# Kernel tuning notes

Hardware: AMD Instinct MI355X
Metric: run time of the kernel (lower is better)

The kernel has to match this reference:

```python
import jax, jax.numpy as jnp
import numpy as np

G = 56      # voxel grid side
N = 60000   # active voxels
K = 27      # 3x3x3 kernel offsets
CIN, COUT = 64, 96


def _build_kernel_map(seed=0):
    """Host-side hash-map neighbor search (what spnn does internally).
    Returns in_idx/out_idx of shape (K, N); padded entries have out_idx == N
    (scattered into a trash row) and in_idx == 0 (any valid gather index)."""
    rng = np.random.default_rng(seed)
    flat = rng.choice(G ** 3, size=N, replace=False)
    coords = np.stack(np.unravel_index(flat, (G, G, G)), axis=1)  # (N, 3)
    lut = -np.ones(G ** 3, dtype=np.int64)
    lut[flat] = np.arange(N)
    offs = np.array([(dx, dy, dz) for dx in (-1, 0, 1)
                     for dy in (-1, 0, 1) for dz in (-1, 0, 1)])
    in_idx = np.zeros((K, N), dtype=np.int32)
    out_idx = np.full((K, N), N, dtype=np.int32)
    for k in range(K):
        nb = coords + offs[k]
        ok = np.all((nb >= 0) & (nb < G), axis=1)
        fl = np.clip(nb[:, 0] * G * G + nb[:, 1] * G + nb[:, 2], 0, G ** 3 - 1)
        j = np.where(ok, lut[fl], -1)
        sel = np.nonzero(j >= 0)[0]
        m = sel.shape[0]
        out_idx[k, :m] = sel.astype(np.int32)       # output point i
        in_idx[k, :m] = j[sel].astype(np.int32)     # its neighbor at offset k
    return jnp.asarray(in_idx), jnp.asarray(out_idx)


def setup_inputs() -> dict:
    key = jax.random.key(0)
    ks = jax.random.split(key, 10)
    in_idx, out_idx = _build_kernel_map(0)
    s1 = 1.0 / np.sqrt(K * CIN)
    s2 = 1.0 / np.sqrt(K * COUT)
    return {
        "x":  jax.random.normal(ks[0], (N, CIN), jnp.float32),
        "W1": jax.random.normal(ks[1], (K, CIN, COUT), jnp.float32) * s1,
        "g1": jnp.ones((COUT,), jnp.float32),
        "b1": jnp.zeros((COUT,), jnp.float32),
        "m1": jax.random.normal(ks[2], (COUT,), jnp.float32) * 0.1,
        "v1": jax.random.uniform(ks[3], (COUT,), jnp.float32, 0.5, 1.5),
        "W2": jax.random.normal(ks[4], (K, COUT, COUT), jnp.float32) * s2,
        "g2": jnp.ones((COUT,), jnp.float32),
        "b2": jnp.zeros((COUT,), jnp.float32),
        "m2": jax.random.normal(ks[5], (COUT,), jnp.float32) * 0.1,
        "v2": jax.random.uniform(ks[6], (COUT,), jnp.float32, 0.5, 1.5),
        "Wd": jax.random.normal(ks[7], (CIN, COUT), jnp.float32) / np.sqrt(CIN),
        "gd": jnp.ones((COUT,), jnp.float32),
        "bd": jnp.zeros((COUT,), jnp.float32),
        "md": jax.random.normal(ks[8], (COUT,), jnp.float32) * 0.1,
        "vd": jax.random.uniform(ks[9], (COUT,), jnp.float32, 0.5, 1.5),
        "in_idx": in_idx,
        "out_idx": out_idx,
    }


def _bn(h, g, b, m, v, eps=1e-5):
    return (h - m) * (g * jax.lax.rsqrt(v + eps)) + b


def _sparse_conv(feat, W, in_idx, out_idx):
    # gather -> GEMM -> scatter-add, one pass per kernel offset.
    n = feat.shape[0]
    out = jnp.zeros((n + 1, W.shape[2]), feat.dtype)  # row n = trash row
    for k in range(W.shape[0]):
        out = out.at[out_idx[k]].add(feat[in_idx[k]] @ W[k])
    return out[:n]


def reference(x, W1, g1, b1, m1, v1, W2, g2, b2, m2, v2,
              Wd, gd, bd, md, vd, in_idx, out_idx):
    h = jax.nn.relu(_bn(_sparse_conv(x, W1, in_idx, out_idx), g1, b1, m1, v1))
    h = _bn(_sparse_conv(h, W2, in_idx, out_idx), g2, b2, m2, v2)
    skip = _bn(x @ Wd, gd, bd, md, vd)  # 1x1 conv downsample (inc != outc)
    return jax.nn.relu(h + skip)
```

## Files before the change

### kernel.cpp

```cpp
#include <hip/hip_runtime.h>


typedef __attribute__((ext_vector_type(8))) short bf16x8;
typedef __attribute__((ext_vector_type(4))) float f32x4;
typedef unsigned short u16;

constexpr int K27  = 27;
constexpr int CIN  = 64;
constexpr int COUT = 96;

#define MFMA __builtin_amdgcn_mfma_f32_16x16x32_bf16

__device__ __forceinline__ u16 f2bf(float f) {
  unsigned u = __float_as_uint(f);
  return (u16)((u + 0x7FFFu + ((u >> 16) & 1u)) >> 16);
}

__device__ __forceinline__ int posf(int c) {
  return ((c >> 2) & 3) * 8 + (c & 3) + ((c >> 4) & 1) * 4;
}

__device__ __forceinline__ bf16x8 ld16(const u16* p) {
  union { bf16x8 f; uint4 u; } r;
  r.u = *reinterpret_cast<const uint4*>(p);
  return r.f;
}

template <int NS>
__device__ __forceinline__ void stageB(const u16* g, u16* l, int t) {
#pragma unroll
  for (int s = 0; s < NS; ++s) {
    __builtin_amdgcn_global_load_lds(
        (const __attribute__((address_space(1))) unsigned int*)(g + s * 2048 + t * 8),
        (__attribute__((address_space(3))) unsigned int*)(l + s * 2048 + t * 8),
        16, 0, 0);
  }
}

__global__ void build_nbT(const int* __restrict__ in_idx, const int* __restrict__ out_idx,
                          int* __restrict__ nbT, int N, int N_pad) {
  int t = blockIdx.x * blockDim.x + threadIdx.x;
  if (t >= K27 * N) return;
  int k = t / N;
  int o = out_idx[t];
  if (o < N) nbT[(size_t)k * N_pad + o] = in_idx[t];
}

__global__ void prep_all(
    const float* __restrict__ x, const float* __restrict__ W1,
    const float* __restrict__ W2, const float* __restrict__ Wd,
    const float* g1, const float* b1, const float* m1, const float* v1,
    const float* g2, const float* b2, const float* m2, const float* v2,
    const float* gd, const float* bd, const float* md, const float* vd,
    u16* __restrict__ xbf, u16* __restrict__ W1t, u16* __restrict__ W2t,
    u16* __restrict__ Wdt, float* __restrict__ bnc, u16* __restrict__ hbf, int N) {
  long i = (long)blockIdx.x * blockDim.x + threadIdx.x;
  const long R0 = (long)(N + 1) * CIN;
  const long R1 = (long)K27 * CIN * COUT;
  const long R2 = (long)K27 * COUT * COUT;
  const long R3 = (long)CIN * COUT;
  if (i < R0) {
    int c = (int)(i & 63);
    float v = (i < (long)N * CIN) ? x[i] : 0.f;
    xbf[(i & ~63L) + (c & 32) + posf(c & 31)] = f2bf(v);
    return;
  }
  i -= R0;
  if (i < R1) {
    int k = (int)(i / (CIN * COUT)), rem = (int)(i % (CIN * COUT));
    int ci = rem / COUT, co = rem % COUT;
    int cidx = (ci & 32) + posf(ci & 31);
    W1t[(size_t)k * 6144 + co * 64 + (cidx ^ ((co & 7) << 3))] = f2bf(W1[i]);
    return;
  }
  i -= R1;
  if (i < R2) {
    int k = (int)(i / (COUT * COUT)), rem = (int)(i % (COUT * COUT));
    int ci = rem / COUT, co = rem % COUT;
    int cidx = (ci >> 5) * 32 + posf(ci & 31);
    W2t[(size_t)k * 12288 + co * 128 + (cidx ^ ((co & 7) << 3))] = f2bf(W2[i]);
    return;
  }
  i -= R2;
  if (i < R3) {
    int ci = (int)(i / COUT), co = (int)(i % COUT);
    Wdt[co * CIN + (ci & 32) + posf(ci & 31)] = f2bf(Wd[i]);
    return;
  }
  i -= R3;
  if (i < COUT) {
    int c = (int)i;
    float A1 = g1[c] * rsqrtf(v1[c] + 1e-5f);
    float A2 = g2[c] * rsqrtf(v2[c] + 1e-5f);
    float Ad = gd[c] * rsqrtf(vd[c] + 1e-5f);
    bnc[c]       = A1;
    bnc[96 + c]  = b1[c] - m1[c] * A1;
    bnc[192 + c] = A2;
    bnc[288 + c] = b2[c] - m2[c] * A2 + bd[c] - md[c] * Ad;
    bnc[384 + c] = Ad / A2;
    hbf[(size_t)N * COUT + c] = 0;
  }
}

__global__ __launch_bounds__(256, 2) void conv1_mfma(
    const u16* __restrict__ xbf, const u16* __restrict__ W1t,
    const int* __restrict__ nbT, const float* __restrict__ bnc,
    u16* __restrict__ hbf, int N, int N_pad) {
  __shared__ u16 Blds[2][6144];
  const int t    = threadIdx.x;
  const int lane = t & 63;
  const int m    = lane & 15;
  const int slot = lane >> 4;
  const int so   = slot * 8;
  const int sw   = (m & 7) << 3;
  const int row0 = blockIdx.x * 64 + (t >> 6) * 16;

  f32x4 acc[6];
#pragma unroll
  for (int n = 0; n < 6; ++n) acc[n] = (f32x4){0.f, 0.f, 0.f, 0.f};

  const int* nbp = nbT + row0 + m;

  stageB<3>(W1t, Blds[0], t);
  int j1 = nbp[N_pad];
  int j2 = nbp[2 * (size_t)N_pad];
  bf16x8 Aa[2], Ab[2];
  {
    int j0 = nbp[0];
    const u16* p = xbf + (size_t)(j0 < 0 ? N : j0) * CIN + so;
    Aa[0] = ld16(p); Aa[1] = ld16(p + 32);
  }
  __syncthreads();

  auto step = [&](int k, bf16x8 (&Ac)[2], bf16x8 (&An)[2]) {
    const int cur = k & 1;
    if (k + 1 < K27) stageB<3>(W1t + (size_t)(k + 1) * 6144, Blds[cur ^ 1], t);
    int jn = j1; j1 = j2;
    j2 = (k + 3 < K27) ? nbp[(size_t)(k + 3) * N_pad] : 0;
    if (k + 1 < K27) {
      const u16* p = xbf + (size_t)(jn < 0 ? N : jn) * CIN + so;
      An[0] = ld16(p); An[1] = ld16(p + 32);
    }
    const u16* Bb = Blds[cur];
#pragma unroll
    for (int c = 0; c < 2; ++c)
#pragma unroll
      for (int n = 0; n < 6; ++n) {
        bf16x8 B = ld16(Bb + n * 1024 + m * 64 + ((c * 32 + so) ^ sw));
        acc[n] = MFMA(Ac[c], B, acc[n], 0, 0, 0);
      }
    __syncthreads();
  };

  for (int kk = 0; kk < K27 - 1; kk += 2) {
    step(kk, Aa, Ab);
    step(kk + 1, Ab, Aa);
  }
  step(K27 - 1, Aa, Ab);

  const int pbase = ((m >> 2) << 3) + (m & 3);
#pragma unroll
  for (int n = 0; n < 6; ++n) {
    const int col  = n * 16 + m;
    const int dcol = (n >> 1) * 32 + pbase + ((n & 1) << 2);
    const float s = bnc[col], b = bnc[COUT + col];
#pragma unroll
    for (int r = 0; r < 4; ++r) {
      const int row = row0 + slot * 4 + r;
      if (row < N)
        hbf[(size_t)row * COUT + dcol] = f2bf(fmaxf(fmaf(acc[n][r], s, b), 0.f));
    }
  }
}

__global__ __launch_bounds__(256, 2) void conv2_mfma(
    const u16* __restrict__ hbf, const u16* __restrict__ W2t,
    const u16* __restrict__ xbf, const u16* __restrict__ Wdt,
    const int* __restrict__ nbT, const float* __restrict__ bnc,
    float* __restrict__ out, int N, int N_pad) {
  __shared__ u16 Blds[2][12288];
  const int t    = threadIdx.x;
  const int lane = t & 63;
  const int m    = lane & 15;
  const int slot = lane >> 4;
  const int so   = slot * 8;
  const int sw   = (m & 7) << 3;
  const int row0 = blockIdx.x * 64 + (t >> 6) * 16;

  f32x4 acc[6];
#pragma unroll
  for (int n = 0; n < 6; ++n) acc[n] = (f32x4){0.f, 0.f, 0.f, 0.f};

  stageB<6>(W2t, Blds[0], t);

  {
    int r0 = row0 + m;
    const u16* p = xbf + (size_t)(r0 < N ? r0 : N) * CIN + so;
    bf16x8 S0 = ld16(p), S1 = ld16(p + 32);
    const u16* wd = Wdt + m * CIN + so;
#pragma unroll
    for (int n = 0; n < 6; ++n) {
      bf16x8 B0 = ld16(wd + n * (16 * CIN));
      bf16x8 B1 = ld16(wd + n * (16 * CIN) + 32);
      acc[n] = MFMA(S0, B0, acc[n], 0, 0, 0);
      acc[n] = MFMA(S1, B1, acc[n], 0, 0, 0);
    }
#pragma unroll
    for (int n = 0; n < 6; ++n) acc[n] *= bnc[384 + n * 16 + m];
  }

  const int* nbp = nbT + row0 + m;
  int j1 = nbp[N_pad];
  int j2 = nbp[2 * (size_t)N_pad];
  bf16x8 Aa[3], Ab[3];
  {
    int j0 = nbp[0];
    const u16* p = hbf + (size_t)(j0 < 0 ? N : j0) * COUT + so;
    Aa[0] = ld16(p); Aa[1] = ld16(p + 32); Aa[2] = ld16(p + 64);
  }
  __syncthreads();

  auto step = [&](int k, bf16x8 (&Ac)[3], bf16x8 (&An)[3]) {
    const int cur = k & 1;
    if (k + 1 < K27) stageB<6>(W2t + (size_t)(k + 1) * 12288, Blds[cur ^ 1], t);
    int jn = j1; j1 = j2;
    j2 = (k + 3 < K27) ? nbp[(size_t)(k + 3) * N_pad] : 0;
    if (k + 1 < K27) {
      const u16* p = hbf + (size_t)(jn < 0 ? N : jn) * COUT + so;
      An[0] = ld16(p); An[1] = ld16(p + 32); An[2] = ld16(p + 64);
    }
    const u16* Bb = Blds[cur];
#pragma unroll
    for (int c = 0; c < 3; ++c)
#pragma unroll
      for (int n = 0; n < 6; ++n) {
        bf16x8 B = ld16(Bb + n * 2048 + m * 128 + ((c * 32 + so) ^ sw));
        acc[n] = MFMA(Ac[c], B, acc[n], 0, 0, 0);
      }
    __syncthreads();
  };

  for (int kk = 0; kk < K27 - 1; kk += 2) {
    step(kk, Aa, Ab);
    step(kk + 1, Ab, Aa);
  }
  step(K27 - 1, Aa, Ab);

#pragma unroll
  for (int n = 0; n < 6; ++n) {
    const int col = n * 16 + m;
    const float s = bnc[192 + col], b = bnc[288 + col];
#pragma unroll
    for (int r = 0; r < 4; ++r) {
      const int row = row0 + slot * 4 + r;
      if (row < N)
        out[(size_t)row * COUT + col] = fmaxf(fmaf(acc[n][r], s, b), 0.f);
    }
  }
}

extern "C" void kernel_launch(void* const* d_in, const int* in_sizes, int n_in,
                              void* d_out, int out_size, void* d_ws, size_t ws_size,
                              hipStream_t stream) {
  const float* x  = (const float*)d_in[0];
  const float* W1 = (const float*)d_in[1];
  const float* g1 = (const float*)d_in[2];
  const float* b1 = (const float*)d_in[3];
  const float* m1 = (const float*)d_in[4];
  const float* v1 = (const float*)d_in[5];
  const float* W2 = (const float*)d_in[6];
  const float* g2 = (const float*)d_in[7];
  const float* b2 = (const float*)d_in[8];
  const float* m2 = (const float*)d_in[9];
  const float* v2 = (const float*)d_in[10];
  const float* Wd = (const float*)d_in[11];
  const float* gd = (const float*)d_in[12];
  const float* bd = (const float*)d_in[13];
  const float* md = (const float*)d_in[14];
  const float* vd = (const float*)d_in[15];
  const int* in_idx  = (const int*)d_in[16];
  const int* out_idx = (const int*)d_in[17];

  const int N  = in_sizes[0] / CIN;
  const int GB = (N + 63) / 64;
  const int N_pad = GB * 64;

  char* ws = (char*)d_ws;
  size_t off = 0;
  auto alloc = [&](size_t bytes) { size_t o = off; off = (off + bytes + 255) & ~(size_t)255; return o; };
  int*   nbT = (int*)(ws + alloc((size_t)K27 * N_pad * sizeof(int)));
  u16*   xbf = (u16*)(ws + alloc((size_t)(N + 1) * CIN * sizeof(u16)));
  u16*   hbf = (u16*)(ws + alloc((size_t)(N + 1) * COUT * sizeof(u16)));
  u16*   W1t = (u16*)(ws + alloc((size_t)K27 * 6144 * sizeof(u16)));
  u16*   W2t = (u16*)(ws + alloc((size_t)K27 * 12288 * sizeof(u16)));
  u16*   Wdt = (u16*)(ws + alloc((size_t)COUT * CIN * sizeof(u16)));
  float* bnc = (float*)(ws + alloc(5 * 96 * sizeof(float)));

  hipMemsetAsync(nbT, 0xFF, (size_t)K27 * N_pad * sizeof(int), stream);
  build_nbT<<<(K27 * N + 255) / 256, 256, 0, stream>>>(in_idx, out_idx, nbT, N, N_pad);

  long ptotal = (long)(N + 1) * CIN + (long)K27 * CIN * COUT +
                (long)K27 * COUT * COUT + (long)CIN * COUT + COUT;
  prep_all<<<(int)((ptotal + 255) / 256), 256, 0, stream>>>(
      x, W1, W2, Wd, g1, b1, m1, v1, g2, b2, m2, v2, gd, bd, md, vd,
      xbf, W1t, W2t, Wdt, bnc, hbf, N);

  conv1_mfma<<<GB, 256, 0, stream>>>(xbf, W1t, nbT, bnc, hbf, N, N_pad);
  conv2_mfma<<<GB, 256, 0, stream>>>(hbf, W2t, xbf, Wdt, nbT, bnc, (float*)d_out, N, N_pad);
}
```

Measured before the change: 125.1 us.

## Retile conv waves to 2x2 grid, prepack weights in MFMA fragment order, XCD-swizzle blocks

Each wave now computes 32 rows by 48 columns instead of 16 rows by 96 columns, so every B fragment read from LDS feeds two MFMAs and LDS traffic per MFMA halves. Weights are prepacked per offset in exact lane-fragment order, removing the XOR swizzle addressing and shrinking W2 staging from 12288 to 9216 elements (no padding). Block indices are remapped across XCDs so neighbouring row blocks share an L2. In exchange, each wave does twice the gather loads per step and holds more registers for A fragments.

```diff
diff --git a/kernel.cpp b/kernel.cpp
--- a/kernel.cpp
+++ b/kernel.cpp
@@ -8,6 +8,8 @@
 constexpr int K27  = 27;
 constexpr int CIN  = 64;
 constexpr int COUT = 96;
+constexpr int W1SZ = 6144;
+constexpr int W2SZ = 9216;
 
 #define MFMA __builtin_amdgcn_mfma_f32_16x16x32_bf16
 
@@ -26,15 +28,27 @@
   return r.f;
 }
 
-template <int NS>
-__device__ __forceinline__ void stageB(const u16* g, u16* l, int t) {
-#pragma unroll
-  for (int s = 0; s < NS; ++s) {
-    __builtin_amdgcn_global_load_lds(
-        (const __attribute__((address_space(1))) unsigned int*)(g + s * 2048 + t * 8),
-        (__attribute__((address_space(3))) unsigned int*)(l + s * 2048 + t * 8),
-        16, 0, 0);
-  }
+__device__ __forceinline__ void gll(const u16* g, u16* l) {
+  __builtin_amdgcn_global_load_lds(
+      (const __attribute__((address_space(1))) unsigned int*)g,
+      (__attribute__((address_space(3))) unsigned int*)l, 16, 0, 0);
+}
+
+__device__ __forceinline__ void stage1(const u16* g, u16* l, int t) {
+#pragma unroll
+  for (int s = 0; s < 3; ++s) gll(g + s * 2048 + t * 8, l + s * 2048 + t * 8);
+}
+
+__device__ __forceinline__ void stage2(const u16* g, u16* l, int t) {
+#pragma unroll
+  for (int s = 0; s < 4; ++s) gll(g + s * 2048 + t * 8, l + s * 2048 + t * 8);
+  if (t < 128) gll(g + 8192 + t * 8, l + 8192 + t * 8);
+}
+
+__device__ __forceinline__ int xcd_swz(int bid, int nblk) {
+  int q = nblk >> 3, r = nblk & 7;
+  int x = bid & 7, i = bid >> 3;
+  return (x < r ? x * (q + 1) : r * (q + 1) + (x - r) * q) + i;
 }
 
 __global__ void build_nbT(const int* __restrict__ in_idx, const int* __restrict__ out_idx,
@@ -56,8 +70,8 @@
     u16* __restrict__ Wdt, float* __restrict__ bnc, u16* __restrict__ hbf, int N) {
   long i = (long)blockIdx.x * blockDim.x + threadIdx.x;
   const long R0 = (long)(N + 1) * CIN;
-  const long R1 = (long)K27 * CIN * COUT;
-  const long R2 = (long)K27 * COUT * COUT;
+  const long R1 = (long)K27 * W1SZ;
+  const long R2 = (long)K27 * W2SZ;
   const long R3 = (long)CIN * COUT;
   if (i < R0) {
     int c = (int)(i & 63);
@@ -67,18 +81,22 @@
   }
   i -= R0;
   if (i < R1) {
-    int k = (int)(i / (CIN * COUT)), rem = (int)(i % (CIN * COUT));
-    int ci = rem / COUT, co = rem % COUT;
-    int cidx = (ci & 32) + posf(ci & 31);
-    W1t[(size_t)k * 6144 + co * 64 + (cidx ^ ((co & 7) << 3))] = f2bf(W1[i]);
+    int k = (int)(i / W1SZ), r = (int)(i % W1SZ);
+    int f = r >> 9, lane = (r >> 3) & 63, j = r & 7;
+    int c = f / 6, n = f % 6, m = lane & 15, g = lane >> 4;
+    int co = n * 16 + m;
+    int ci = c * 32 + 4 * g + (j & 3) + 16 * (j >> 2);
+    W1t[i] = f2bf(W1[((size_t)k * CIN + ci) * COUT + co]);
     return;
   }
   i -= R1;
   if (i < R2) {
-    int k = (int)(i / (COUT * COUT)), rem = (int)(i % (COUT * COUT));
-    int ci = rem / COUT, co = rem % COUT;
-    int cidx = (ci >> 5) * 32 + posf(ci & 31);
-    W2t[(size_t)k * 12288 + co * 128 + (cidx ^ ((co & 7) << 3))] = f2bf(W2[i]);
+    int k = (int)(i / W2SZ), r = (int)(i % W2SZ);
+    int f = r >> 9, lane = (r >> 3) & 63, j = r & 7;
+    int c = f / 6, n = f % 6, m = lane & 15, g = lane >> 4;
+    int co = n * 16 + m;
+    int ci = c * 32 + 4 * g + (j & 3) + 16 * (j >> 2);
+    W2t[i] = f2bf(W2[((size_t)k * COUT + ci) * COUT + co]);
     return;
   }
   i -= R2;
@@ -106,48 +124,62 @@
     const u16* __restrict__ xbf, const u16* __restrict__ W1t,
     const int* __restrict__ nbT, const float* __restrict__ bnc,
     u16* __restrict__ hbf, int N, int N_pad) {
-  __shared__ u16 Blds[2][6144];
+  __shared__ u16 Blds[2][W1SZ];
   const int t    = threadIdx.x;
   const int lane = t & 63;
   const int m    = lane & 15;
   const int slot = lane >> 4;
   const int so   = slot * 8;
-  const int sw   = (m & 7) << 3;
-  const int row0 = blockIdx.x * 64 + (t >> 6) * 16;
-
-  f32x4 acc[6];
-#pragma unroll
-  for (int n = 0; n < 6; ++n) acc[n] = (f32x4){0.f, 0.f, 0.f, 0.f};
-
-  const int* nbp = nbT + row0 + m;
-
-  stageB<3>(W1t, Blds[0], t);
-  int j1 = nbp[N_pad];
-  int j2 = nbp[2 * (size_t)N_pad];
-  bf16x8 Aa[2], Ab[2];
+  const int wid  = t >> 6;
+  const int wr   = wid >> 1;
+  const int wc   = wid & 1;
+  const int bswz = xcd_swz(blockIdx.x, gridDim.x);
+  const int roww = bswz * 64 + wr * 32;
+
+  f32x4 acc[2][3];
+#pragma unroll
+  for (int s = 0; s < 2; ++s)
+#pragma unroll
+    for (int n = 0; n < 3; ++n) acc[s][n] = (f32x4){0.f, 0.f, 0.f, 0.f};
+
+  const int* nbp = nbT + roww + m;
+
+  stage1(W1t, Blds[0], t);
+  int j1a = nbp[N_pad],               j1b = nbp[N_pad + 16];
+  int j2a = nbp[2 * (size_t)N_pad],   j2b = nbp[2 * (size_t)N_pad + 16];
+  bf16x8 Aa[2][2], Ab[2][2];
   {
-    int j0 = nbp[0];
-    const u16* p = xbf + (size_t)(j0 < 0 ? N : j0) * CIN + so;
-    Aa[0] = ld16(p); Aa[1] = ld16(p + 32);
+    int j0a = nbp[0], j0b = nbp[16];
+    const u16* pa = xbf + (size_t)(j0a < 0 ? N : j0a) * CIN + so;
+    const u16* pb = xbf + (size_t)(j0b < 0 ? N : j0b) * CIN + so;
+    Aa[0][0] = ld16(pa); Aa[0][1] = ld16(pa + 32);
+    Aa[1][0] = ld16(pb); Aa[1][1] = ld16(pb + 32);
   }
   __syncthreads();
 
-  auto step = [&](int k, bf16x8 (&Ac)[2], bf16x8 (&An)[2]) {
+  auto step = [&](int k, bf16x8 (&Ac)[2][2], bf16x8 (&An)[2][2]) {
     const int cur = k & 1;
-    if (k + 1 < K27) stageB<3>(W1t + (size_t)(k + 1) * 6144, Blds[cur ^ 1], t);
-    int jn = j1; j1 = j2;
-    j2 = (k + 3 < K27) ? nbp[(size_t)(k + 3) * N_pad] : 0;
+    if (k + 1 < K27) stage1(W1t + (size_t)(k + 1) * W1SZ, Blds[cur ^ 1], t);
+    int j3a = 0, j3b = 0;
+    if (k + 3 < K27) {
+      j3a = nbp[(size_t)(k + 3) * N_pad];
+      j3b = nbp[(size_t)(k + 3) * N_pad + 16];
+    }
     if (k + 1 < K27) {
-      const u16* p = xbf + (size_t)(jn < 0 ? N : jn) * CIN + so;
-      An[0] = ld16(p); An[1] = ld16(p + 32);
-    }
-    const u16* Bb = Blds[cur];
+      const u16* pa = xbf + (size_t)(j1a < 0 ? N : j1a) * CIN + so;
+      const u16* pb = xbf + (size_t)(j1b < 0 ? N : j1b) * CIN + so;
+      An[0][0] = ld16(pa); An[0][1] = ld16(pa + 32);
+      An[1][0] = ld16(pb); An[1][1] = ld16(pb + 32);
+    }
+    j1a = j2a; j1b = j2b; j2a = j3a; j2b = j3b;
+    const u16* Bb = Blds[cur] + wc * 1536 + lane * 8;
 #pragma unroll
     for (int c = 0; c < 2; ++c)
 #pragma unroll
-      for (int n = 0; n < 6; ++n) {
-        bf16x8 B = ld16(Bb + n * 1024 + m * 64 + ((c * 32 + so) ^ sw));
-        acc[n] = MFMA(Ac[c], B, acc[n], 0, 0, 0);
+      for (int nn = 0; nn < 3; ++nn) {
+        bf16x8 B = ld16(Bb + (c * 6 + nn) * 512);
+        acc[0][nn] = MFMA(Ac[0][c], B, acc[0][nn], 0, 0, 0);
+        acc[1][nn] = MFMA(Ac[1][c], B, acc[1][nn], 0, 0, 0);
       }
     __syncthreads();
   };
@@ -160,16 +192,19 @@
 
   const int pbase = ((m >> 2) << 3) + (m & 3);
 #pragma unroll
-  for (int n = 0; n < 6; ++n) {
-    const int col  = n * 16 + m;
+  for (int nn = 0; nn < 3; ++nn) {
+    const int n   = wc * 3 + nn;
+    const int col = n * 16 + m;
     const int dcol = (n >> 1) * 32 + pbase + ((n & 1) << 2);
-    const float s = bnc[col], b = bnc[COUT + col];
-#pragma unroll
-    for (int r = 0; r < 4; ++r) {
-      const int row = row0 + slot * 4 + r;
-      if (row < N)
-        hbf[(size_t)row * COUT + dcol] = f2bf(fmaxf(fmaf(acc[n][r], s, b), 0.f));
-    }
+    const float sc = bnc[col], bi = bnc[COUT + col];
+#pragma unroll
+    for (int s = 0; s < 2; ++s)
+#pragma unroll
+      for (int r = 0; r < 4; ++r) {
+        const int row = roww + s * 16 + slot * 4 + r;
+        if (row < N)
+          hbf[(size_t)row * COUT + dcol] = f2bf(fmaxf(fmaf(acc[s][nn][r], sc, bi), 0.f));
+      }
   }
 }
 
@@ -178,64 +213,86 @@
     const u16* __restrict__ xbf, const u16* __restrict__ Wdt,
     const int* __restrict__ nbT, const float* __restrict__ bnc,
     float* __restrict__ out, int N, int N_pad) {
-  __shared__ u16 Blds[2][12288];
+  __shared__ u16 Blds[2][W2SZ];
   const int t    = threadIdx.x;
   const int lane = t & 63;
   const int m    = lane & 15;
   const int slot = lane >> 4;
   const int so   = slot * 8;
-  const int sw   = (m & 7) << 3;
-  const int row0 = blockIdx.x * 64 + (t >> 6) * 16;
-
-  f32x4 acc[6];
-#pragma unroll
-  for (int n = 0; n < 6; ++n) acc[n] = (f32x4){0.f, 0.f, 0.f, 0.f};
-
-  stageB<6>(W2t, Blds[0], t);
+  const int wid  = t >> 6;
+  const int wr   = wid >> 1;
+  const int wc   = wid & 1;
+  const int bswz = xcd_swz(blockIdx.x, gridDim.x);
+  const int roww = bswz * 64 + wr * 32;
+
+  f32x4 acc[2][3];
+#pragma unroll
+  for (int s = 0; s < 2; ++s)
+#pragma unroll
+    for (int n = 0; n < 3; ++n) acc[s][n] = (f32x4){0.f, 0.f, 0.f, 0.f};
+
+  stage2(W2t, Blds[0], t);
 
   {
-    int r0 = row0 + m;
-    const u16* p = xbf + (size_t)(r0 < N ? r0 : N) * CIN + so;
-    bf16x8 S0 = ld16(p), S1 = ld16(p + 32);
-    const u16* wd = Wdt + m * CIN + so;
-#pragma unroll
-    for (int n = 0; n < 6; ++n) {
-      bf16x8 B0 = ld16(wd + n * (16 * CIN));
-      bf16x8 B1 = ld16(wd + n * (16 * CIN) + 32);
-      acc[n] = MFMA(S0, B0, acc[n], 0, 0, 0);
-      acc[n] = MFMA(S1, B1, acc[n], 0, 0, 0);
-    }
-#pragma unroll
-    for (int n = 0; n < 6; ++n) acc[n] *= bnc[384 + n * 16 + m];
-  }
-
-  const int* nbp = nbT + row0 + m;
-  int j1 = nbp[N_pad];
-  int j2 = nbp[2 * (size_t)N_pad];
-  bf16x8 Aa[3], Ab[3];
+    int r0 = roww + m, r1 = roww + 16 + m;
+    const u16* pa = xbf + (size_t)(r0 < N ? r0 : N) * CIN + so;
+    const u16* pb = xbf + (size_t)(r1 < N ? r1 : N) * CIN + so;
+    bf16x8 S0a = ld16(pa), S1a = ld16(pa + 32);
+    bf16x8 S0b = ld16(pb), S1b = ld16(pb + 32);
+#pragma unroll
+    for (int nn = 0; nn < 3; ++nn) {
+      const int col = (wc * 3 + nn) * 16 + m;
+      const u16* wd = Wdt + col * CIN + so;
+      bf16x8 B0 = ld16(wd), B1 = ld16(wd + 32);
+      acc[0][nn] = MFMA(S0a, B0, acc[0][nn], 0, 0, 0);
+      acc[0][nn] = MFMA(S1a, B1, acc[0][nn], 0, 0, 0);
+      acc[1][nn] = MFMA(S0b, B0, acc[1][nn], 0, 0, 0);
+      acc[1][nn] = MFMA(S1b, B1, acc[1][nn], 0, 0, 0);
+    }
+#pragma unroll
+    for (int nn = 0; nn < 3; ++nn) {
+      float rr = bnc[384 + (wc * 3 + nn) * 16 + m];
+      acc[0][nn] *= rr;
+      acc[1][nn] *= rr;
+    }
+  }
+
+  const int* nbp = nbT + roww + m;
+  int j1a = nbp[N_pad],             j1b = nbp[N_pad + 16];
+  int j2a = nbp[2 * (size_t)N_pad], j2b = nbp[2 * (size_t)N_pad + 16];
+  bf16x8 Aa[2][3], Ab[2][3];
   {
-    int j0 = nbp[0];
-    const u16* p = hbf + (size_t)(j0 < 0 ? N : j0) * COUT + so;
-    Aa[0] = ld16(p); Aa[1] = ld16(p + 32); Aa[2] = ld16(p + 64);
+    int j0a = nbp[0], j0b = nbp[16];
+    const u16* pa = hbf + (size_t)(j0a < 0 ? N : j0a) * COUT + so;
+    const u16* pb = hbf + (size_t)(j0b < 0 ? N : j0b) * COUT + so;
+    Aa[0][0] = ld16(pa); Aa[0][1] = ld16(pa + 32); Aa[0][2] = ld16(pa + 64);
+    Aa[1][0] = ld16(pb); Aa[1][1] = ld16(pb + 32); Aa[1][2] = ld16(pb + 64);
   }
   __syncthreads();
 
-  auto step = [&](int k, bf16x8 (&Ac)[3], bf16x8 (&An)[3]) {
+  auto step = [&](int k, bf16x8 (&Ac)[2][3], bf16x8 (&An)[2][3]) {
     const int cur = k & 1;
-    if (k + 1 < K27) stageB<6>(W2t + (size_t)(k + 1) * 12288, Blds[cur ^ 1], t);
-    int jn = j1; j1 = j2;
-    j2 = (k + 3 < K27) ? nbp[(size_t)(k + 3) * N_pad] : 0;
+    if (k + 1 < K27) stage2(W2t + (size_t)(k + 1) * W2SZ, Blds[cur ^ 1], t);
+    int j3a = 0, j3b = 0;
+    if (k + 3 < K27) {
+      j3a = nbp[(size_t)(k + 3) * N_pad];
+      j3b = nbp[(size_t)(k + 3) * N_pad + 16];
+    }
     if (k + 1 < K27) {
-      const u16* p = hbf + (size_t)(jn < 0 ? N : jn) * COUT + so;
-      An[0] = ld16(p); An[1] = ld16(p + 32); An[2] = ld16(p + 64);
-    }
-    const u16* Bb = Blds[cur];
+      const u16* pa = hbf + (size_t)(j1a < 0 ? N : j1a) * COUT + so;
+      const u16* pb = hbf + (size_t)(j1b < 0 ? N : j1b) * COUT + so;
+      An[0][0] = ld16(pa); An[0][1] = ld16(pa + 32); An[0][2] = ld16(pa + 64);
+      An[1][0] = ld16(pb); An[1][1] = ld16(pb + 32); An[1][2] = ld16(pb + 64);
+    }
+    j1a = j2a; j1b = j2b; j2a = j3a; j2b = j3b;
+    const u16* Bb = Blds[cur] + wc * 1536 + lane * 8;
 #pragma unroll
     for (int c = 0; c < 3; ++c)
 #pragma unroll
-      for (int n = 0; n < 6; ++n) {
-        bf16x8 B = ld16(Bb + n * 2048 + m * 128 + ((c * 32 + so) ^ sw));
-        acc[n] = MFMA(Ac[c], B, acc[n], 0, 0, 0);
+      for (int nn = 0; nn < 3; ++nn) {
+        bf16x8 B = ld16(Bb + (c * 6 + nn) * 512);
+        acc[0][nn] = MFMA(Ac[0][c], B, acc[0][nn], 0, 0, 0);
+        acc[1][nn] = MFMA(Ac[1][c], B, acc[1][nn], 0, 0, 0);
       }
     __syncthreads();
   };
@@ -247,15 +304,17 @@
   step(K27 - 1, Aa, Ab);
 
 #pragma unroll
-  for (int n = 0; n < 6; ++n) {
-    const int col = n * 16 + m;
-    const float s = bnc[192 + col], b = bnc[288 + col];
-#pragma unroll
-    for (int r = 0; r < 4; ++r) {
-      const int row = row0 + slot * 4 + r;
-      if (row < N)
-        out[(size_t)row * COUT + col] = fmaxf(fmaf(acc[n][r], s, b), 0.f);
-    }
+  for (int nn = 0; nn < 3; ++nn) {
+    const int col = (wc * 3 + nn) * 16 + m;
+    const float sc = bnc[192 + col], bi = bnc[288 + col];
+#pragma unroll
+    for (int s = 0; s < 2; ++s)
+#pragma unroll
+      for (int r = 0; r < 4; ++r) {
+        const int row = roww + s * 16 + slot * 4 + r;
+        if (row < N)
+          out[(size_t)row * COUT + col] = fmaxf(fmaf(acc[s][nn][r], sc, bi), 0.f);
+      }
   }
 }
 
@@ -291,16 +350,16 @@
   int*   nbT = (int*)(ws + alloc((size_t)K27 * N_pad * sizeof(int)));
   u16*   xbf = (u16*)(ws + alloc((size_t)(N + 1) * CIN * sizeof(u16)));
   u16*   hbf = (u16*)(ws + alloc((size_t)(N + 1) * COUT * sizeof(u16)));
-  u16*   W1t = (u16*)(ws + alloc((size_t)K27 * 6144 * sizeof(u16)));
-  u16*   W2t = (u16*)(ws + alloc((size_t)K27 * 12288 * sizeof(u16)));
+  u16*   W1t = (u16*)(ws + alloc((size_t)K27 * W1SZ * sizeof(u16)));
+  u16*   W2t = (u16*)(ws + alloc((size_t)K27 * W2SZ * sizeof(u16)));
   u16*   Wdt = (u16*)(ws + alloc((size_t)COUT * CIN * sizeof(u16)));
   float* bnc = (float*)(ws + alloc(5 * 96 * sizeof(float)));
 
   hipMemsetAsync(nbT, 0xFF, (size_t)K27 * N_pad * sizeof(int), stream);
   build_nbT<<<(K27 * N + 255) / 256, 256, 0, stream>>>(in_idx, out_idx, nbT, N, N_pad);
 
-  long ptotal = (long)(N + 1) * CIN + (long)K27 * CIN * COUT +
-                (long)K27 * COUT * COUT + (long)CIN * COUT + COUT;
+  long ptotal = (long)(N + 1) * CIN + (long)K27 * W1SZ + (long)K27 * W2SZ +
+                (long)CIN * COUT + COUT;
   prep_all<<<(int)((ptotal + 255) / 256), 256, 0, stream>>>(
       x, W1, W2, Wd, g1, b1, m1, v1, g2, b2, m2, v2, gd, bd, md, vd,
       xbf, W1t, W2t, Wdt, bnc, hbf, N);
```

New measurement: 136.5 us. 9.1% more time.
